# Kernel optimization log

Measured on AMD Instinct MI355X. Metric: run time of the kernel, lower is better.

## Reference

```python
import jax, jax.numpy as jnp
import numpy as np

WINDOW_SIZE = 64  # matches module init

def setup_inputs() -> dict:
    key = jax.random.key(0)
    kq, kk, kv = jax.random.split(key, 3)
    B, S, H, D = 1, 2048, 8, 64
    return {
        "query": jax.random.normal(kq, (B, S, H, D), dtype=jnp.float32),
        "key": jax.random.normal(kk, (B, S, H, D), dtype=jnp.float32),
        "value": jax.random.normal(kv, (B, S, H, D), dtype=jnp.float32),
    }

def reference(query, key, value):
    # Sliding-window (sparse) attention, window [i-w, i+w] inclusive.
    B, S, H, D = query.shape
    w = WINDOW_SIZE
    scale = 1.0 / jnp.sqrt(jnp.float32(D))
    offs = jnp.arange(-w, w + 1)                      # [W], W = 2w+1
    idx = jnp.arange(S)[:, None] + offs[None, :]      # [S, W]
    valid = (idx >= 0) & (idx < S)                    # [S, W]
    idx_c = jnp.clip(idx, 0, S - 1)
    k_win = key[:, idx_c]                             # [B, S, W, H, D]
    v_win = value[:, idx_c]                           # [B, S, W, H, D]
    scores = jnp.einsum('bshd,bswhd->bshw', query * scale, k_win)
    scores = jnp.where(valid[None, :, None, :], scores, -jnp.inf)
    attn = jax.nn.softmax(scores, axis=-1)            # [B, S, H, W]
    out = jnp.einsum('bshw,bswhd->bshd', attn, v_win)
    return out
```

## Files before the change

kernel.cpp:

```cpp
#include <hip/hip_runtime.h>
#include <stdint.h>

#define S_LEN 2048
#define NH 8
#define HD 64
#define W 64
#define TQ 32
#define ROWS 160
#define LDK 68

__device__ __forceinline__ float rdlane(float v, int l) {
  return __int_as_float(__builtin_amdgcn_readlane(__float_as_int(v), l));
}
__device__ __forceinline__ float b2f(uint16_t v) {
  return __uint_as_float(((uint32_t)v) << 16);
}
__device__ __forceinline__ uint16_t f2b(float f) {
  uint32_t u = __float_as_uint(f);
  u += 0x7FFFu + ((u >> 16) & 1u);
  return (uint16_t)(u >> 16);
}
__device__ __forceinline__ float wave_max(float v) {
#pragma unroll
  for (int m = 32; m >= 1; m >>= 1) v = fmaxf(v, __shfl_xor(v, m, 64));
  return v;
}
__device__ __forceinline__ float wave_sum(float v) {
#pragma unroll
  for (int m = 32; m >= 1; m >>= 1) v += __shfl_xor(v, m, 64);
  return v;
}

__global__ __launch_bounds__(256, 2)
void swa_kernel(const float* __restrict__ Q, const float* __restrict__ K,
                const float* __restrict__ V, float* __restrict__ O) {
  __shared__ float    Ks[ROWS * LDK];
  __shared__ uint16_t Vs[ROWS * HD];

  const int tile = blockIdx.x;
  const int h    = blockIdx.y;
  const int tid  = threadIdx.x;
  const int g0   = tile * TQ - W;

#pragma unroll
  for (int it = 0; it < 10; ++it) {
    int idx = tid + it * 256;
    int row = idx >> 4;
    int c   = idx & 15;
    int g   = g0 + row;
    float4 kv = make_float4(0.f, 0.f, 0.f, 0.f);
    float4 vv = make_float4(0.f, 0.f, 0.f, 0.f);
    if ((unsigned)g < (unsigned)S_LEN) {
      const float* kp = K + ((g * NH + h) << 6) + (c << 2);
      const float* vp = V + ((g * NH + h) << 6) + (c << 2);
      kv = *(const float4*)kp;
      vv = *(const float4*)vp;
    }
    *(float4*)&Ks[row * LDK + (c << 2)] = kv;
    ushort4 pk;
    pk.x = f2b(vv.x); pk.y = f2b(vv.y); pk.z = f2b(vv.z); pk.w = f2b(vv.w);
    *(ushort4*)&Vs[row * HD + (c << 2)] = pk;
  }
  __syncthreads();

  const int lane = tid & 63;
  const int qb   = (tid >> 6) * 8;
  const int s0   = tile * TQ + qb;

  float qv[8];
#pragma unroll
  for (int i = 0; i < 8; ++i)
    qv[i] = Q[(((s0 + i) * NH + h) << 6) + lane] * 0.125f;

  const float* ka = &Ks[(qb + lane) * LDK];
  const float* kb = &Ks[(qb + 64 + lane) * LDK];
  int rc = qb + 128 + lane; if (rc > ROWS - 1) rc = ROWS - 1;
  const float* kc = &Ks[rc * LDK];

  float sa[8], sb[8], sc[8];
#pragma unroll
  for (int i = 0; i < 8; ++i) { sa[i] = 0.f; sb[i] = 0.f; sc[i] = 0.f; }

#pragma unroll 4
  for (int d = 0; d < 64; d += 4) {
    float4 A  = *(const float4*)(ka + d);
    float4 Bv = *(const float4*)(kb + d);
    float4 Cv = *(const float4*)(kc + d);
#pragma unroll
    for (int i = 0; i < 8; ++i) {
      float q0 = rdlane(qv[i], d + 0);
      float q1 = rdlane(qv[i], d + 1);
      float q2 = rdlane(qv[i], d + 2);
      float q3 = rdlane(qv[i], d + 3);
      sa[i] = fmaf(q0, A.x,  sa[i]); sa[i] = fmaf(q1, A.y,  sa[i]);
      sa[i] = fmaf(q2, A.z,  sa[i]); sa[i] = fmaf(q3, A.w,  sa[i]);
      sb[i] = fmaf(q0, Bv.x, sb[i]); sb[i] = fmaf(q1, Bv.y, sb[i]);
      sb[i] = fmaf(q2, Bv.z, sb[i]); sb[i] = fmaf(q3, Bv.w, sb[i]);
      sc[i] = fmaf(q0, Cv.x, sc[i]); sc[i] = fmaf(q1, Cv.y, sc[i]);
      sc[i] = fmaf(q2, Cv.z, sc[i]); sc[i] = fmaf(q3, Cv.w, sc[i]);
    }
  }

  float ea[8], eb[8], ec[8], rsum[8];
#pragma unroll
  for (int i = 0; i < 8; ++i) {
    bool va = (lane >= i) && ((s0 - 64 + lane) >= 0);
    bool vb = (s0 + lane) < S_LEN;
    bool vc = (lane <= i) && ((s0 + 64 + lane) < S_LEN);
    float m3 = fmaxf(fmaxf(va ? sa[i] : -INFINITY, vb ? sb[i] : -INFINITY),
                     vc ? sc[i] : -INFINITY);
    float mx = wave_max(m3);
    ea[i] = va ? __expf(sa[i] - mx) : 0.f;
    eb[i] = vb ? __expf(sb[i] - mx) : 0.f;
    ec[i] = vc ? __expf(sc[i] - mx) : 0.f;
    float sm = wave_sum(ea[i] + eb[i] + ec[i]);
    rsum[i] = 1.0f / sm;
  }

  float acc[8];
#pragma unroll
  for (int i = 0; i < 8; ++i) acc[i] = 0.f;

  const uint16_t* vpa = &Vs[qb * HD + lane];
#pragma unroll 4
  for (int j = 0; j < 64; ++j) {
    float vv = b2f(vpa[j * HD]);
#pragma unroll
    for (int i = 0; i < 8; ++i) acc[i] = fmaf(rdlane(ea[i], j), vv, acc[i]);
  }
  const uint16_t* vpb = vpa + 64 * HD;
#pragma unroll 4
  for (int j = 0; j < 64; ++j) {
    float vv = b2f(vpb[j * HD]);
#pragma unroll
    for (int i = 0; i < 8; ++i) acc[i] = fmaf(rdlane(eb[i], j), vv, acc[i]);
  }
  const uint16_t* vpc = vpa + 128 * HD;
#pragma unroll
  for (int j = 0; j < 8; ++j) {
    float vv = b2f(vpc[j * HD]);
#pragma unroll
    for (int i = 0; i < 8; ++i) acc[i] = fmaf(rdlane(ec[i], j), vv, acc[i]);
  }

#pragma unroll
  for (int i = 0; i < 8; ++i)
    O[(((s0 + i) * NH + h) << 6) + lane] = acc[i] * rsum[i];
}

extern "C" void kernel_launch(void* const* d_in, const int* in_sizes, int n_in,
                              void* d_out, int out_size, void* d_ws, size_t ws_size,
                              hipStream_t stream) {
  const float* Q = (const float*)d_in[0];
  const float* K = (const float*)d_in[1];
  const float* V = (const float*)d_in[2];
  float* O = (float*)d_out;
  dim3 grid(S_LEN / TQ, NH);
  swa_kernel<<<grid, 256, 0, stream>>>(Q, K, V, O);
}
```

Before: 91.35 us.

## Rewrite sliding-window attention with bf16 MFMA for QK and PV

```diff
diff --git a/kernel.cpp b/kernel.cpp
--- a/kernel.cpp
+++ b/kernel.cpp
@@ -2,23 +2,28 @@
 #include <stdint.h>
 
 #define S_LEN 2048
-#define NH 8
-#define HD 64
-#define W 64
-#define TQ 32
-#define ROWS 160
-#define LDK 68
+#define NH    8
+#define TQ    32
+#define NKV   160
+#define SS    161
+#define PP    168
+#define PVT   168
 
-__device__ __forceinline__ float rdlane(float v, int l) {
-  return __int_as_float(__builtin_amdgcn_readlane(__float_as_int(v), l));
-}
-__device__ __forceinline__ float b2f(uint16_t v) {
-  return __uint_as_float(((uint32_t)v) << 16);
-}
+typedef __attribute__((ext_vector_type(8))) short  short8;
+typedef __attribute__((ext_vector_type(4))) float  floatx4;
+
 __device__ __forceinline__ uint16_t f2b(float f) {
   uint32_t u = __float_as_uint(f);
   u += 0x7FFFu + ((u >> 16) & 1u);
   return (uint16_t)(u >> 16);
+}
+__device__ __forceinline__ short8 pack8(float4 a, float4 b) {
+  short8 r;
+  r[0] = (short)f2b(a.x); r[1] = (short)f2b(a.y);
+  r[2] = (short)f2b(a.z); r[3] = (short)f2b(a.w);
+  r[4] = (short)f2b(b.x); r[5] = (short)f2b(b.y);
+  r[6] = (short)f2b(b.z); r[7] = (short)f2b(b.w);
+  return r;
 }
 __device__ __forceinline__ float wave_max(float v) {
 #pragma unroll
@@ -32,120 +37,127 @@
 }
 
 __global__ __launch_bounds__(256, 2)
-void swa_kernel(const float* __restrict__ Q, const float* __restrict__ K,
-                const float* __restrict__ V, float* __restrict__ O) {
-  __shared__ float    Ks[ROWS * LDK];
-  __shared__ uint16_t Vs[ROWS * HD];
+void swa_mfma(const float* __restrict__ Q, const float* __restrict__ K,
+              const float* __restrict__ V, float* __restrict__ O) {
+  __shared__ float    Ssc[TQ * SS];
+  __shared__ uint16_t Pw [TQ * PP];
+  __shared__ uint16_t Vt [64 * PVT];
 
   const int tile = blockIdx.x;
   const int h    = blockIdx.y;
   const int tid  = threadIdx.x;
-  const int g0   = tile * TQ - W;
+  const int g0   = tile * TQ - 64;
 
 #pragma unroll
   for (int it = 0; it < 10; ++it) {
-    int idx = tid + it * 256;
-    int row = idx >> 4;
-    int c   = idx & 15;
-    int g   = g0 + row;
-    float4 kv = make_float4(0.f, 0.f, 0.f, 0.f);
-    float4 vv = make_float4(0.f, 0.f, 0.f, 0.f);
-    if ((unsigned)g < (unsigned)S_LEN) {
-      const float* kp = K + ((g * NH + h) << 6) + (c << 2);
-      const float* vp = V + ((g * NH + h) << 6) + (c << 2);
-      kv = *(const float4*)kp;
-      vv = *(const float4*)vp;
+    int task = tid + it * 256;
+    int d    = task & 63;
+    int cq   = task >> 6;
+    int gb   = g0 + (cq << 2);
+    float v[4];
+#pragma unroll
+    for (int k = 0; k < 4; ++k) {
+      int g = gb + k;
+      g = g < 0 ? 0 : (g > S_LEN - 1 ? S_LEN - 1 : g);
+      v[k] = V[((g * NH + h) << 6) + d];
     }
-    *(float4*)&Ks[row * LDK + (c << 2)] = kv;
-    ushort4 pk;
-    pk.x = f2b(vv.x); pk.y = f2b(vv.y); pk.z = f2b(vv.z); pk.w = f2b(vv.w);
-    *(ushort4*)&Vs[row * HD + (c << 2)] = pk;
+    uint32_t p01 = (uint32_t)f2b(v[0]) | ((uint32_t)f2b(v[1]) << 16);
+    uint32_t p23 = (uint32_t)f2b(v[2]) | ((uint32_t)f2b(v[3]) << 16);
+    uint32_t* dst = (uint32_t*)&Vt[d * PVT + (cq << 2)];
+    dst[0] = p01; dst[1] = p23;
+  }
+
+  const int lane = tid & 63;
+  const int w    = tid >> 6;
+  const int r16  = lane & 15;
+  const int quad = lane >> 4;
+  const int m    = w & 1;
+  const int n0   = w >> 1;
+
+  const int qrow = tile * TQ + m * 16 + r16;
+  const float* qb = Q + ((qrow * NH + h) << 6) + (quad << 3);
+  float4 q0 = *(const float4*)(qb);
+  float4 q1 = *(const float4*)(qb + 4);
+  float4 q2 = *(const float4*)(qb + 32);
+  float4 q3 = *(const float4*)(qb + 36);
+  const float sc = 0.125f;
+  q0.x*=sc;q0.y*=sc;q0.z*=sc;q0.w*=sc;  q1.x*=sc;q1.y*=sc;q1.z*=sc;q1.w*=sc;
+  q2.x*=sc;q2.y*=sc;q2.z*=sc;q2.w*=sc;  q3.x*=sc;q3.y*=sc;q3.z*=sc;q3.w*=sc;
+  short8 aq0 = pack8(q0, q1);
+  short8 aq1 = pack8(q2, q3);
+
+#pragma unroll
+  for (int u = 0; u < 5; ++u) {
+    int nt = n0 + 2 * u;
+    int g  = g0 + nt * 16 + r16;
+    g = g < 0 ? 0 : (g > S_LEN - 1 ? S_LEN - 1 : g);
+    const float* kb = K + ((g * NH + h) << 6) + (quad << 3);
+    float4 k0 = *(const float4*)(kb);
+    float4 k1 = *(const float4*)(kb + 4);
+    float4 k2 = *(const float4*)(kb + 32);
+    float4 k3 = *(const float4*)(kb + 36);
+    short8 b0 = pack8(k0, k1);
+    short8 b1 = pack8(k2, k3);
+    floatx4 acc = {0.f, 0.f, 0.f, 0.f};
+    acc = __builtin_amdgcn_mfma_f32_16x16x32_bf16(aq0, b0, acc, 0, 0, 0);
+    acc = __builtin_amdgcn_mfma_f32_16x16x32_bf16(aq1, b1, acc, 0, 0, 0);
+    int colbase = nt * 16 + r16;
+    int rowbase = m * 16 + quad * 4;
+#pragma unroll
+    for (int rg = 0; rg < 4; ++rg)
+      Ssc[(rowbase + rg) * SS + colbase] = acc[rg];
   }
   __syncthreads();
 
-  const int lane = tid & 63;
-  const int qb   = (tid >> 6) * 8;
-  const int s0   = tile * TQ + qb;
+#pragma unroll
+  for (int k = 0; k < 8; ++k) {
+    int r  = w * 8 + k;
+    int lo = r;
+    int t0 = 64 - tile * TQ;  if (t0 > lo) lo = t0;
+    int hi = r + 128;
+    int t1 = (S_LEN - 1) - g0; if (t1 < hi) hi = t1;
+    const float* Sr = &Ssc[r * SS];
+    int c0 = lane, c1 = lane + 64, c2 = lane + 128;
+    int c2c = c2 > 160 ? 160 : c2;
+    float s0v = Sr[c0], s1v = Sr[c1], s2v = Sr[c2c];
+    bool v0 = (c0 >= lo) && (c0 <= hi);
+    bool v1 = (c1 >= lo) && (c1 <= hi);
+    bool v2 = (c2 >= lo) && (c2 <= hi);
+    float mx = wave_max(fmaxf(fmaxf(v0 ? s0v : -INFINITY, v1 ? s1v : -INFINITY),
+                              v2 ? s2v : -INFINITY));
+    float e0 = v0 ? __expf(s0v - mx) : 0.f;
+    float e1 = v1 ? __expf(s1v - mx) : 0.f;
+    float e2 = v2 ? __expf(s2v - mx) : 0.f;
+    float rs = 1.0f / wave_sum(e0 + e1 + e2);
+    uint16_t* Pr = &Pw[r * PP];
+    Pr[c0]  = f2b(e0 * rs);
+    Pr[c1]  = f2b(e1 * rs);
+    Pr[c2c] = f2b(e2 * rs);
+  }
+  __syncthreads();
 
-  float qv[8];
+  short8 pa[5];
+  const uint16_t* Prow = &Pw[(m * 16 + r16) * PP + (quad << 3)];
 #pragma unroll
-  for (int i = 0; i < 8; ++i)
-    qv[i] = Q[(((s0 + i) * NH + h) << 6) + lane] * 0.125f;
-
-  const float* ka = &Ks[(qb + lane) * LDK];
-  const float* kb = &Ks[(qb + 64 + lane) * LDK];
-  int rc = qb + 128 + lane; if (rc > ROWS - 1) rc = ROWS - 1;
-  const float* kc = &Ks[rc * LDK];
-
-  float sa[8], sb[8], sc[8];
-#pragma unroll
-  for (int i = 0; i < 8; ++i) { sa[i] = 0.f; sb[i] = 0.f; sc[i] = 0.f; }
-
-#pragma unroll 4
-  for (int d = 0; d < 64; d += 4) {
-    float4 A  = *(const float4*)(ka + d);
-    float4 Bv = *(const float4*)(kb + d);
-    float4 Cv = *(const float4*)(kc + d);
-#pragma unroll
-    for (int i = 0; i < 8; ++i) {
-      float q0 = rdlane(qv[i], d + 0);
-      float q1 = rdlane(qv[i], d + 1);
-      float q2 = rdlane(qv[i], d + 2);
-      float q3 = rdlane(qv[i], d + 3);
-      sa[i] = fmaf(q0, A.x,  sa[i]); sa[i] = fmaf(q1, A.y,  sa[i]);
-      sa[i] = fmaf(q2, A.z,  sa[i]); sa[i] = fmaf(q3, A.w,  sa[i]);
-      sb[i] = fmaf(q0, Bv.x, sb[i]); sb[i] = fmaf(q1, Bv.y, sb[i]);
-      sb[i] = fmaf(q2, Bv.z, sb[i]); sb[i] = fmaf(q3, Bv.w, sb[i]);
-      sc[i] = fmaf(q0, Cv.x, sc[i]); sc[i] = fmaf(q1, Cv.y, sc[i]);
-      sc[i] = fmaf(q2, Cv.z, sc[i]); sc[i] = fmaf(q3, Cv.w, sc[i]);
-    }
-  }
-
-  float ea[8], eb[8], ec[8], rsum[8];
-#pragma unroll
-  for (int i = 0; i < 8; ++i) {
-    bool va = (lane >= i) && ((s0 - 64 + lane) >= 0);
-    bool vb = (s0 + lane) < S_LEN;
-    bool vc = (lane <= i) && ((s0 + 64 + lane) < S_LEN);
-    float m3 = fmaxf(fmaxf(va ? sa[i] : -INFINITY, vb ? sb[i] : -INFINITY),
-                     vc ? sc[i] : -INFINITY);
-    float mx = wave_max(m3);
-    ea[i] = va ? __expf(sa[i] - mx) : 0.f;
-    eb[i] = vb ? __expf(sb[i] - mx) : 0.f;
-    ec[i] = vc ? __expf(sc[i] - mx) : 0.f;
-    float sm = wave_sum(ea[i] + eb[i] + ec[i]);
-    rsum[i] = 1.0f / sm;
-  }
-
-  float acc[8];
-#pragma unroll
-  for (int i = 0; i < 8; ++i) acc[i] = 0.f;
-
-  const uint16_t* vpa = &Vs[qb * HD + lane];
-#pragma unroll 4
-  for (int j = 0; j < 64; ++j) {
-    float vv = b2f(vpa[j * HD]);
-#pragma unroll
-    for (int i = 0; i < 8; ++i) acc[i] = fmaf(rdlane(ea[i], j), vv, acc[i]);
-  }
-  const uint16_t* vpb = vpa + 64 * HD;
-#pragma unroll 4
-  for (int j = 0; j < 64; ++j) {
-    float vv = b2f(vpb[j * HD]);
-#pragma unroll
-    for (int i = 0; i < 8; ++i) acc[i] = fmaf(rdlane(eb[i], j), vv, acc[i]);
-  }
-  const uint16_t* vpc = vpa + 128 * HD;
-#pragma unroll
-  for (int j = 0; j < 8; ++j) {
-    float vv = b2f(vpc[j * HD]);
-#pragma unroll
-    for (int i = 0; i < 8; ++i) acc[i] = fmaf(rdlane(ec[i], j), vv, acc[i]);
-  }
+  for (int kq = 0; kq < 5; ++kq)
+    pa[kq] = *(const short8*)(Prow + kq * 32);
 
 #pragma unroll
-  for (int i = 0; i < 8; ++i)
-    O[(((s0 + i) * NH + h) << 6) + lane] = acc[i] * rsum[i];
+  for (int t = 0; t < 2; ++t) {
+    int nt = n0 + 2 * t;
+    const uint16_t* Vrow = &Vt[(nt * 16 + r16) * PVT + (quad << 3)];
+    floatx4 o = {0.f, 0.f, 0.f, 0.f};
+#pragma unroll
+    for (int kq = 0; kq < 5; ++kq) {
+      short8 bv = *(const short8*)(Vrow + kq * 32);
+      o = __builtin_amdgcn_mfma_f32_16x16x32_bf16(pa[kq], bv, o, 0, 0, 0);
+    }
+    int orow = tile * TQ + m * 16 + quad * 4;
+    int d    = nt * 16 + r16;
+#pragma unroll
+    for (int rg = 0; rg < 4; ++rg)
+      O[(((orow + rg) * NH + h) << 6) + d] = o[rg];
+  }
 }
 
 extern "C" void kernel_launch(void* const* d_in, const int* in_sizes, int n_in,
@@ -156,5 +168,5 @@
   const float* V = (const float*)d_in[2];
   float* O = (float*)d_out;
   dim3 grid(S_LEN / TQ, NH);
-  swa_kernel<<<grid, 256, 0, stream>>>(Q, K, V, O);
+  swa_mfma<<<grid, 256, 0, stream>>>(Q, K, V, O);
 }
```

New measurement: 79.35 us. 1.15x faster.
